# Kernel optimization log

Measured on AMD Instinct MI355X. Metric: run time of the kernel, lower is better.

The kernel has to match this reference:

```python
import jax, jax.numpy as jnp
import numpy as np

S_DIM = 128            # attention head width s
E_DIM = 1024           # expansion e = 2*hidden
SQRT_S = 128.0 ** 0.5
EPS = 1e-5


def setup_inputs() -> dict:
    key = jax.random.key(0)
    ks = jax.random.split(key, 8)
    B, S, H = 64, 512, 512
    uv_dim = 2 * E_DIM + S_DIM  # 2176
    # xavier-uniform-ish scale for uv weight
    lim = (6.0 / (H + uv_dim)) ** 0.5
    return {
        "x": jax.random.normal(ks[0], (B, S, H), dtype=jnp.float32),
        "ln_g": jnp.ones((1,), dtype=jnp.float32),
        "uv_w": jax.random.uniform(ks[1], (uv_dim, H), minval=-lim, maxval=lim, dtype=jnp.float32),
        "uv_b": jnp.zeros((uv_dim,), dtype=jnp.float32),
        "gamma": jax.random.uniform(ks[2], (2, S_DIM), dtype=jnp.float32),
        "beta": jax.random.uniform(ks[3], (2, S_DIM), dtype=jnp.float32),
        "w_bias": jax.random.uniform(ks[4], (2 * S - 1,), dtype=jnp.float32),
        "o_w": jax.random.normal(ks[5], (H, E_DIM), dtype=jnp.float32) * 0.02,
        "o_b": jnp.zeros((H,), dtype=jnp.float32),
    }


def _rope(x):
    # x: [B, S, 2, s]; rotate along the sequence dim (dim=1)
    S = x.shape[1]
    half = x.shape[-1] // 2
    pos = jnp.arange(S, dtype=jnp.float32)
    # torch: freq_seq = -arange(half)/half; inv_freq = 10000**(-freq_seq)
    inv_freq = 10000.0 ** (jnp.arange(half, dtype=jnp.float32) / half)
    sinus = pos[:, None, None] * inv_freq[None, None, :]  # [S, 1, half]
    sin, cos = jnp.sin(sinus), jnp.cos(sinus)
    x1, x2 = x[..., :half], x[..., half:]
    return jnp.concatenate([x1 * cos - x2 * sin, x2 * cos + x1 * sin], axis=-1)


def reference(x, ln_g, uv_w, uv_b, gamma, beta, w_bias, o_w, o_b):
    B, S, H = x.shape
    # ScaleNorm
    norm = jnp.linalg.norm(x, axis=-1, keepdims=True) * (H ** -0.5)
    xn = x / jnp.maximum(norm, EPS) * ln_g
    # fused uv projection + SiLU
    act = jax.nn.silu(xn @ uv_w.T + uv_b)  # [B, S, 2e+s]
    u = act[..., :E_DIM]
    v = act[..., E_DIM:2 * E_DIM]
    base = act[..., 2 * E_DIM:]                      # [B, S, s]
    base = base[:, :, None, :] * gamma + beta        # [B, S, 2, s]
    base = _rope(base)
    q, k = base[:, :, 0, :], base[:, :, 1, :]
    # scores + relative position bias: bias[i, j] = w[j - i + S - 1]
    qk = jnp.einsum('bsd,btd->bst', q, k)
    idx = jnp.arange(S)[None, :] - jnp.arange(S)[:, None] + (S - 1)
    qk = qk + w_bias[idx]
    # relu2 similarity kernel
    kernel = jnp.square(jax.nn.relu(qk / SQRT_S))    # [B, S, S]
    out = u * jnp.einsum('bst,bte->bse', kernel, v)  # gated attention
    out = out @ o_w.T + o_b
    return out + x  # use_shortcut: hidden == output
```

## Files before the change

kernel.cpp:

```cpp
#include <hip/hip_runtime.h>
#include <math.h>


#define M_TOT   32768
#define S_LEN   512
#define H_DIM   512
#define E_DIMC  1024
#define UV_DIM  2176
#define D_DIM   128

using floatx4  = __attribute__((ext_vector_type(4))) float;
using uintx2   = __attribute__((ext_vector_type(2))) unsigned int;
using uintx4   = __attribute__((ext_vector_type(4))) unsigned int;
using ushortx4 = __attribute__((ext_vector_type(4))) unsigned short;
using short8   = __attribute__((ext_vector_type(8))) short;

#define ASYNC_CP16(gsrc, ldst)                                                  \
    __builtin_amdgcn_global_load_lds(                                           \
        (const __attribute__((address_space(1))) void*)(gsrc),                  \
        (__attribute__((address_space(3))) void*)(ldst), 16, 0, 0)

__device__ __forceinline__ float bf2f(unsigned short h) {
    union { unsigned int u; float f; } c;
    c.u = ((unsigned int)h) << 16;
    return c.f;
}
__device__ __forceinline__ unsigned short f2bf(float f) {
    union { float f; unsigned int u; } c;
    c.f = f;
    unsigned int r = c.u + 0x7fffu + ((c.u >> 16) & 1u);
    return (unsigned short)(r >> 16);
}
__device__ __forceinline__ float silu_fast(float x) {
    float e = __expf(-x);
    return x * __builtin_amdgcn_rcpf(1.0f + e);
}

__global__ __launch_bounds__(256) void f2bf_kernel(const float* __restrict__ in,
                                                   unsigned short* __restrict__ out,
                                                   int n4) {
    int i = blockIdx.x * 256 + threadIdx.x;
    if (i < n4) {
        floatx4 v = ((const floatx4*)in)[i];
        ushortx4 o;
        o.x = f2bf(v.x); o.y = f2bf(v.y); o.z = f2bf(v.z); o.w = f2bf(v.w);
        ((ushortx4*)out)[i] = o;
    }
}

__global__ __launch_bounds__(256) void rmsnorm_kernel(const float* __restrict__ x,
                                                      const float* __restrict__ ln_g,
                                                      unsigned short* __restrict__ xn) {
    int row  = blockIdx.x * 4 + (threadIdx.x >> 6);
    int lane = threadIdx.x & 63;
    const float* xr = x + (size_t)row * H_DIM;
    floatx4 v0 = ((const floatx4*)xr)[lane];
    floatx4 v1 = ((const floatx4*)xr)[lane + 64];
    float ss = v0.x*v0.x + v0.y*v0.y + v0.z*v0.z + v0.w*v0.w
             + v1.x*v1.x + v1.y*v1.y + v1.z*v1.z + v1.w*v1.w;
    #pragma unroll
    for (int off = 32; off > 0; off >>= 1) ss += __shfl_xor(ss, off, 64);
    float norm = sqrtf(ss) * 0.044194173824159216f;
    float sc   = ln_g[0] / fmaxf(norm, 1e-5f);
    unsigned short* xo = xn + (size_t)row * H_DIM;
    ushortx4 o0, o1;
    o0.x = f2bf(v0.x * sc); o0.y = f2bf(v0.y * sc);
    o0.z = f2bf(v0.z * sc); o0.w = f2bf(v0.w * sc);
    o1.x = f2bf(v1.x * sc); o1.y = f2bf(v1.y * sc);
    o1.z = f2bf(v1.z * sc); o1.w = f2bf(v1.w * sc);
    ((ushortx4*)xo)[lane]      = o0;
    ((ushortx4*)xo)[lane + 64] = o1;
}

__global__ __launch_bounds__(64) void rope_table_kernel(float* __restrict__ cost,
                                                        float* __restrict__ sint) {
    int s = blockIdx.x;
    int j = threadIdx.x;
    float invf = (float)pow(10000.0, (double)j / 64.0);
    float ang  = (float)s * invf;
    double a   = (double)ang;
    cost[s * 64 + j] = (float)cos(a);
    sint[s * 64 + j] = (float)sin(a);
}

__global__ __launch_bounds__(256) void rope_apply_kernel(const float* __restrict__ base,
                                                         const float* __restrict__ gamma,
                                                         const float* __restrict__ beta,
                                                         const float* __restrict__ cost,
                                                         const float* __restrict__ sint,
                                                         unsigned short* __restrict__ q,
                                                         unsigned short* __restrict__ k) {
    int idx = blockIdx.x * 256 + threadIdx.x;
    int m = idx >> 6;
    int j = idx & 63;
    int s = m & (S_LEN - 1);
    float b1 = base[(size_t)m * D_DIM + j];
    float b2 = base[(size_t)m * D_DIM + 64 + j];
    float c  = cost[s * 64 + j];
    float sn = sint[s * 64 + j];
    float yq1 = b1 * gamma[j]       + beta[j];
    float yq2 = b2 * gamma[64 + j]  + beta[64 + j];
    float yk1 = b1 * gamma[128 + j] + beta[128 + j];
    float yk2 = b2 * gamma[192 + j] + beta[192 + j];
    q[(size_t)m * D_DIM + j]      = f2bf(yq1 * c - yq2 * sn);
    q[(size_t)m * D_DIM + 64 + j] = f2bf(yq2 * c + yq1 * sn);
    k[(size_t)m * D_DIM + j]      = f2bf(yk1 * c - yk2 * sn);
    k[(size_t)m * D_DIM + 64 + j] = f2bf(yk2 * c + yk1 * sn);
}

struct GemmLds {
    unsigned short As[128 * 64];
    unsigned short Bs[128 * 64];
};

template <bool SWAPT>
__device__ __forceinline__ void gemm_bt_core(const unsigned short* __restrict__ A,
                                             const unsigned short* __restrict__ B,
                                             int lda, int ldb, int K,
                                             int m0, int n0,
                                             GemmLds& lds, floatx4 (&acc)[4][4]) {
    const int tid  = threadIdx.x;
    const int lane = tid & 63;
    const int wave = tid >> 6;
    const int quad = lane >> 4;
    const int l16  = lane & 15;
    const int wm   = (wave >> 1) * 64;
    const int wn   = (wave & 1) * 64;
    const int lrow = lane >> 3;
    const int cgs  = ((lane & 7) ^ lrow) * 8;

    #pragma unroll
    for (int i = 0; i < 4; i++)
        #pragma unroll
        for (int j = 0; j < 4; j++) acc[i][j] = (floatx4){0.f, 0.f, 0.f, 0.f};

    for (int kt = 0; kt < K; kt += 64) {
        #pragma unroll
        for (int i = 0; i < 4; i++) {
            int r0 = wave * 32 + i * 8;
            const unsigned short* ga = A + (size_t)(m0 + r0 + lrow) * lda + kt + cgs;
            const unsigned short* gb = B + (size_t)(n0 + r0 + lrow) * ldb + kt + cgs;
            ASYNC_CP16(ga, &lds.As[r0 * 64]);
            ASYNC_CP16(gb, &lds.Bs[r0 * 64]);
        }
        __syncthreads();
        #pragma unroll
        for (int kk = 0; kk < 64; kk += 32) {
            short8 af[4], bf[4];
            const int pc = (kk + quad * 8) ^ ((l16 & 7) * 8);
            #pragma unroll
            for (int mt = 0; mt < 4; mt++) {
                int row = wm + mt * 16 + l16;
                union { short8 s8; uintx4 u4; } fu;
                fu.u4 = *(const uintx4*)&lds.As[row * 64 + pc];
                af[mt] = fu.s8;
            }
            #pragma unroll
            for (int nt = 0; nt < 4; nt++) {
                int row = wn + nt * 16 + l16;
                union { short8 s8; uintx4 u4; } fu;
                fu.u4 = *(const uintx4*)&lds.Bs[row * 64 + pc];
                bf[nt] = fu.s8;
            }
            #pragma unroll
            for (int mt = 0; mt < 4; mt++)
                #pragma unroll
                for (int nt = 0; nt < 4; nt++)
                    acc[mt][nt] = SWAPT
                        ? __builtin_amdgcn_mfma_f32_16x16x32_bf16(bf[nt], af[mt], acc[mt][nt], 0, 0, 0)
                        : __builtin_amdgcn_mfma_f32_16x16x32_bf16(af[mt], bf[nt], acc[mt][nt], 0, 0, 0);
        }
        __syncthreads();
    }
}

union LdsU {
    GemmLds g;
    unsigned short T[128 * 128];
};
__device__ __forceinline__ int swz(int row, int col) {
    return row * 128 + ((((col >> 3) ^ (row & 7)) << 3) | (col & 7));
}

__global__ __launch_bounds__(256) void gemm1_kernel(const unsigned short* __restrict__ xn,
                                                    const unsigned short* __restrict__ uvw,
                                                    const float* __restrict__ uvb,
                                                    unsigned short* __restrict__ u,
                                                    unsigned short* __restrict__ vT,
                                                    float* __restrict__ base) {
    __shared__ LdsU lds;
    floatx4 acc[4][4];
    const int m0 = blockIdx.x * 128, n0 = blockIdx.y * 128;

    const int tid = threadIdx.x, lane = tid & 63, wave = tid >> 6;
    const int quad = lane >> 4, l16 = lane & 15;
    const int wm = (wave >> 1) * 64, wn = (wave & 1) * 64;

    if (blockIdx.y < 8) {
        gemm_bt_core<true>(xn, uvw, H_DIM, H_DIM, H_DIM, m0, n0, lds.g, acc);
        #pragma unroll
        for (int mt = 0; mt < 4; mt++) {
            int row = wm + mt * 16 + l16;
            #pragma unroll
            for (int nt = 0; nt < 4; nt++) {
                int nl = wn + nt * 16 + quad * 4;
                floatx4 b4 = *(const floatx4*)&uvb[n0 + nl];
                ushortx4 pk;
                #pragma unroll
                for (int r = 0; r < 4; r++)
                    pk[r] = f2bf(silu_fast(acc[mt][nt][r] + b4[r]));
                *(uintx2*)&lds.T[swz(row, nl)] = *(uintx2*)&pk;
            }
        }
        __syncthreads();
        #pragma unroll
        for (int i = 0; i < 8; i++) {
            int idx = tid + i * 256;
            int row = idx >> 4;
            int j   = idx & 15;
            *(uintx4*)(u + (size_t)(m0 + row) * E_DIMC + n0 + j * 8) =
                *(const uintx4*)&lds.T[swz(row, j * 8)];
        }
    } else if (blockIdx.y < 16) {
        gemm_bt_core<false>(xn, uvw, H_DIM, H_DIM, H_DIM, m0, n0, lds.g, acc);
        #pragma unroll
        for (int nt = 0; nt < 4; nt++) {
            int nl = wn + nt * 16 + l16;
            float bias = uvb[n0 + nl];
            #pragma unroll
            for (int mt = 0; mt < 4; mt++) {
                ushortx4 pk;
                #pragma unroll
                for (int r = 0; r < 4; r++)
                    pk[r] = f2bf(silu_fast(acc[mt][nt][r] + bias));
                *(uintx2*)&lds.T[swz(nl, wm + mt * 16 + quad * 4)] = *(uintx2*)&pk;
            }
        }
        __syncthreads();
        const int b   = m0 >> 9;
        const int sg0 = m0 & (S_LEN - 1);
        const int eg0 = n0 - E_DIMC;
        #pragma unroll
        for (int i = 0; i < 8; i++) {
            int idx = tid + i * 256;
            int e   = idx >> 4;
            int j   = idx & 15;
            *(uintx4*)(vT + ((size_t)b * E_DIMC + eg0 + e) * S_LEN + sg0 + j * 8) =
                *(const uintx4*)&lds.T[swz(e, j * 8)];
        }
    } else {
        gemm_bt_core<false>(xn, uvw, H_DIM, H_DIM, H_DIM, m0, n0, lds.g, acc);
        #pragma unroll
        for (int mt = 0; mt < 4; mt++)
            #pragma unroll
            for (int nt = 0; nt < 4; nt++)
                #pragma unroll
                for (int r = 0; r < 4; r++) {
                    int m = m0 + wm + mt * 16 + quad * 4 + r;
                    int n = n0 + wn + nt * 16 + l16;
                    float val = acc[mt][nt][r] + uvb[n];
                    base[(size_t)m * D_DIM + (n - 2 * E_DIMC)] = silu_fast(val);
                }
    }
}

__global__ __launch_bounds__(256) void gemm_qk_kernel(const unsigned short* __restrict__ q,
                                                      const unsigned short* __restrict__ k,
                                                      const float* __restrict__ wbias,
                                                      unsigned short* __restrict__ P) {
    __shared__ LdsU lds;
    floatx4 acc[4][4];
    size_t boff = (size_t)blockIdx.z * S_LEN * D_DIM;
    unsigned short* Pb = P + (size_t)blockIdx.z * S_LEN * S_LEN;
    const int m0 = blockIdx.x * 128, n0 = blockIdx.y * 128;
    gemm_bt_core<true>(q + boff, k + boff, D_DIM, D_DIM, D_DIM, m0, n0, lds.g, acc);

    const int tid = threadIdx.x, lane = tid & 63, wave = tid >> 6;
    const int quad = lane >> 4, l16 = lane & 15;
    const int wm = (wave >> 1) * 64, wn = (wave & 1) * 64;
    #pragma unroll
    for (int mt = 0; mt < 4; mt++) {
        int row = wm + mt * 16 + l16;
        int s   = m0 + row;
        #pragma unroll
        for (int nt = 0; nt < 4; nt++) {
            int nl = wn + nt * 16 + quad * 4;
            int t0 = n0 + nl;
            ushortx4 pk;
            #pragma unroll
            for (int r = 0; r < 4; r++) {
                float z = (acc[mt][nt][r] + wbias[t0 + r - s + (S_LEN - 1)]) * 0.08838834764831845f;
                z = fmaxf(z, 0.f);
                pk[r] = f2bf(z * z);
            }
            *(uintx2*)&lds.T[swz(row, nl)] = *(uintx2*)&pk;
        }
    }
    __syncthreads();
    #pragma unroll
    for (int i = 0; i < 8; i++) {
        int idx = tid + i * 256;
        int row = idx >> 4;
        int j   = idx & 15;
        *(uintx4*)(Pb + (size_t)(m0 + row) * S_LEN + n0 + j * 8) =
            *(const uintx4*)&lds.T[swz(row, j * 8)];
    }
}

__global__ __launch_bounds__(256) void gemm_pv_kernel(const unsigned short* __restrict__ P,
                                                      const unsigned short* __restrict__ vT,
                                                      unsigned short* __restrict__ u) {
    __shared__ LdsU lds;
    floatx4 acc[4][4];
    int bb = blockIdx.z;
    const unsigned short* Pb  = P  + (size_t)bb * S_LEN * S_LEN;
    const unsigned short* vTb = vT + (size_t)bb * E_DIMC * S_LEN;
    const int m0 = blockIdx.x * 128, n0 = blockIdx.y * 128;
    gemm_bt_core<true>(Pb, vTb, S_LEN, S_LEN, S_LEN, m0, n0, lds.g, acc);

    const int tid = threadIdx.x, lane = tid & 63, wave = tid >> 6;
    const int quad = lane >> 4, l16 = lane & 15;
    const int wm = (wave >> 1) * 64, wn = (wave & 1) * 64;
    #pragma unroll
    for (int mt = 0; mt < 4; mt++) {
        int row = wm + mt * 16 + l16;
        #pragma unroll
        for (int nt = 0; nt < 4; nt++) {
            int nl = wn + nt * 16 + quad * 4;
            ushortx4 pk;
            #pragma unroll
            for (int r = 0; r < 4; r++) pk[r] = f2bf(acc[mt][nt][r]);
            *(uintx2*)&lds.T[swz(row, nl)] = *(uintx2*)&pk;
        }
    }
    __syncthreads();
    #pragma unroll
    for (int i = 0; i < 8; i++) {
        int idx = tid + i * 256;
        int row = idx >> 4;
        int j   = idx & 15;
        size_t off = ((size_t)bb * S_LEN + m0 + row) * E_DIMC + n0 + j * 8;
        union { uintx4 u4; unsigned short s[8]; } tv, uv, ov;
        tv.u4 = *(const uintx4*)&lds.T[swz(row, j * 8)];
        uv.u4 = *(const uintx4*)(u + off);
        #pragma unroll
        for (int jj = 0; jj < 8; jj++) ov.s[jj] = f2bf(bf2f(tv.s[jj]) * bf2f(uv.s[jj]));
        *(uintx4*)(u + off) = ov.u4;
    }
}

__global__ __launch_bounds__(256) void gemm_out_kernel(const unsigned short* __restrict__ oe,
                                                       const unsigned short* __restrict__ ow,
                                                       const float* __restrict__ ob,
                                                       const float* __restrict__ x,
                                                       float* __restrict__ out) {
    __shared__ GemmLds lds;
    floatx4 acc[4][4];
    const int m0 = blockIdx.y * 128, n0 = blockIdx.x * 128;
    gemm_bt_core<true>(oe, ow, E_DIMC, E_DIMC, E_DIMC, m0, n0, lds, acc);

    const int tid = threadIdx.x, lane = tid & 63, wave = tid >> 6;
    const int quad = lane >> 4, l16 = lane & 15;
    const int wm = (wave >> 1) * 64, wn = (wave & 1) * 64;

    #pragma unroll
    for (int mt = 0; mt < 4; mt++) {
        int m = m0 + wm + mt * 16 + l16;
        #pragma unroll
        for (int nt = 0; nt < 4; nt++) {
            int n = n0 + wn + nt * 16 + quad * 4;
            size_t off = (size_t)m * H_DIM + n;
            floatx4 b4 = *(const floatx4*)&ob[n];
            floatx4 x4 = *(const floatx4*)&x[off];
            *(floatx4*)&out[off] = acc[mt][nt] + b4 + x4;
        }
    }
}

extern "C" void kernel_launch(void* const* d_in, const int* in_sizes, int n_in,
                              void* d_out, int out_size, void* d_ws, size_t ws_size,
                              hipStream_t stream) {
    const float* x     = (const float*)d_in[0];
    const float* ln_g  = (const float*)d_in[1];
    const float* uv_w  = (const float*)d_in[2];
    const float* uv_b  = (const float*)d_in[3];
    const float* gamma = (const float*)d_in[4];
    const float* beta  = (const float*)d_in[5];
    const float* wbias = (const float*)d_in[6];
    const float* o_w   = (const float*)d_in[7];
    const float* o_b   = (const float*)d_in[8];
    float* out = (float*)d_out;

    char* ws = (char*)d_ws;
    size_t off = 0;
    auto alloc = [&](size_t bytes) {
        void* p = ws + off;
        off += (bytes + 255) & ~(size_t)255;
        return p;
    };
    unsigned short* u     = (unsigned short*)alloc((size_t)M_TOT * E_DIMC * 2);
    unsigned short* vT    = (unsigned short*)alloc((size_t)64 * E_DIMC * S_LEN * 2);
    unsigned short* xn    = (unsigned short*)alloc((size_t)M_TOT * H_DIM * 2);
    unsigned short* P     = xn;
    float*          base  = (float*)alloc((size_t)M_TOT * D_DIM * 4);
    unsigned short* q     = (unsigned short*)alloc((size_t)M_TOT * D_DIM * 2);
    unsigned short* k     = (unsigned short*)alloc((size_t)M_TOT * D_DIM * 2);
    float*          cost  = (float*)alloc((size_t)S_LEN * 64 * 4);
    float*          sint  = (float*)alloc((size_t)S_LEN * 64 * 4);
    unsigned short* uvwb  = (unsigned short*)alloc((size_t)UV_DIM * H_DIM * 2);
    unsigned short* owb   = (unsigned short*)alloc((size_t)H_DIM * E_DIMC * 2);
    (void)ws_size; (void)in_sizes; (void)n_in; (void)out_size;

    f2bf_kernel<<<(UV_DIM * H_DIM / 4 + 255) / 256, 256, 0, stream>>>(uv_w, uvwb, UV_DIM * H_DIM / 4);
    f2bf_kernel<<<(H_DIM * E_DIMC / 4 + 255) / 256, 256, 0, stream>>>(o_w, owb, H_DIM * E_DIMC / 4);
    rope_table_kernel<<<S_LEN, 64, 0, stream>>>(cost, sint);

    rmsnorm_kernel<<<M_TOT / 4, 256, 0, stream>>>(x, ln_g, xn);

    gemm1_kernel<<<dim3(M_TOT / 128, 17), 256, 0, stream>>>(xn, uvwb, uv_b, u, vT, base);

    rope_apply_kernel<<<M_TOT * 64 / 256, 256, 0, stream>>>(base, gamma, beta, cost, sint, q, k);

    gemm_qk_kernel<<<dim3(S_LEN / 128, S_LEN / 128, 64), 256, 0, stream>>>(q, k, wbias, P);

    gemm_pv_kernel<<<dim3(S_LEN / 128, E_DIMC / 128, 64), 256, 0, stream>>>(P, vT, u);

    gemm_out_kernel<<<dim3(H_DIM / 128, M_TOT / 128), 256, 0, stream>>>(u, owb, o_b, x, out);
}
```

Baseline: 398.9 us.

## Use 256x256 tiles with 4-stage async pipeline for projection GEMMs

Replaces the 128x128 uv-projection and output-projection GEMMs with 512-thread kernels computing 256x256 tiles. Each kernel uses a 4-buffer LDS ring filled by async global-to-LDS copies issued two k-steps ahead, plus raised wave priority around the MFMA bursts. The uv weight is zero-padded to 2304 rows so the final base tile fits the 256-wide grid. Larger tiles raise data reuse per LDS load, at the cost of far fewer blocks for the output GEMM (256) and wasted work on the padded base tile.

Result: no change. 393.7 us (-1.3%).

```diff
diff --git a/kernel.cpp b/kernel.cpp
--- a/kernel.cpp
+++ b/kernel.cpp
@@ -7,6 +7,7 @@
 #define H_DIM   512
 #define E_DIMC  1024
 #define UV_DIM  2176
+#define UV_PAD  2304
 #define D_DIM   128
 
 using floatx4  = __attribute__((ext_vector_type(4))) float;
@@ -44,6 +45,22 @@
         floatx4 v = ((const floatx4*)in)[i];
         ushortx4 o;
         o.x = f2bf(v.x); o.y = f2bf(v.y); o.z = f2bf(v.z); o.w = f2bf(v.w);
+        ((ushortx4*)out)[i] = o;
+    }
+}
+
+__global__ __launch_bounds__(256) void f2bf_pad_kernel(const float* __restrict__ in,
+                                                       unsigned short* __restrict__ out,
+                                                       int n4_src, int n4_dst) {
+    int i = blockIdx.x * 256 + threadIdx.x;
+    if (i < n4_dst) {
+        ushortx4 o;
+        if (i < n4_src) {
+            floatx4 v = ((const floatx4*)in)[i];
+            o.x = f2bf(v.x); o.y = f2bf(v.y); o.z = f2bf(v.z); o.w = f2bf(v.w);
+        } else {
+            o.x = 0; o.y = 0; o.z = 0; o.w = 0;
+        }
         ((ushortx4*)out)[i] = o;
     }
 }
@@ -108,6 +125,227 @@
     k[(size_t)m * D_DIM + 64 + j] = f2bf(yk2 * c + yk1 * sn);
 }
 
+template <bool SWAPT>
+__device__ __forceinline__ void gemm256_core(const unsigned short* __restrict__ A,
+                                             const unsigned short* __restrict__ B,
+                                             int lda, int ldb, int K,
+                                             int m0, int n0,
+                                             unsigned short (&st)[4][2][128][64],
+                                             floatx4 (&acc)[8][4]) {
+    const int tid  = threadIdx.x;
+    const int lane = tid & 63;
+    const int wave = tid >> 6;
+    const int quad = lane >> 4;
+    const int l16  = lane & 15;
+    const int wrow = (wave >> 2) * 128;
+    const int wcol = (wave & 3) * 64;
+
+    const int q0    = wave * 128 + lane;
+    const int R0    = q0 >> 3;
+    const int cp0   = q0 & 7;
+    const int c0    = cp0 ^ (R0 & 7);
+    const int srow0 = 2 * R0 + (c0 >> 2);
+    const int scol0 = (c0 & 3) * 8;
+
+    const unsigned short* pa0 = A + (size_t)(m0 + srow0) * lda + scol0;
+    const unsigned short* pa1 = pa0 + (size_t)16 * lda;
+    const unsigned short* pb0 = B + (size_t)(n0 + srow0) * ldb + scol0;
+    const unsigned short* pb1 = pb0 + (size_t)16 * ldb;
+    const int ldsOff0 = (wave * 128) * 8;
+    const int ldsOff1 = (wave * 128 + 64) * 8;
+
+    #pragma unroll
+    for (int i = 0; i < 8; i++)
+        #pragma unroll
+        for (int j = 0; j < 4; j++) acc[i][j] = (floatx4){0.f, 0.f, 0.f, 0.f};
+
+    const int NT = K >> 5;
+    auto stage = [&](int t) {
+        unsigned short* sA = &st[t & 3][0][0][0];
+        unsigned short* sB = &st[t & 3][1][0][0];
+        const int kt = t * 32;
+        ASYNC_CP16(pa0 + kt, sA + ldsOff0);
+        ASYNC_CP16(pa1 + kt, sA + ldsOff1);
+        ASYNC_CP16(pb0 + kt, sB + ldsOff0);
+        ASYNC_CP16(pb1 + kt, sB + ldsOff1);
+    };
+    stage(0);
+    stage(1);
+
+    int aoff[8], boff[4];
+    #pragma unroll
+    for (int mt = 0; mt < 8; mt++) {
+        int r  = wrow + mt * 16 + l16;
+        int Rr = r >> 1;
+        int cp = (((r & 1) << 2) + quad) ^ (Rr & 7);
+        aoff[mt] = Rr * 64 + cp * 8;
+    }
+    #pragma unroll
+    for (int nt = 0; nt < 4; nt++) {
+        int r  = wcol + nt * 16 + l16;
+        int Rr = r >> 1;
+        int cp = (((r & 1) << 2) + quad) ^ (Rr & 7);
+        boff[nt] = Rr * 64 + cp * 8;
+    }
+
+    for (int t = 0; t < NT; ++t) {
+        if (t < NT - 1) asm volatile("s_waitcnt vmcnt(4)" ::: "memory");
+        else            asm volatile("s_waitcnt vmcnt(0)" ::: "memory");
+        __builtin_amdgcn_sched_barrier(0);
+        __builtin_amdgcn_s_barrier();
+        __builtin_amdgcn_sched_barrier(0);
+        if (t + 2 < NT) stage(t + 2);
+
+        const unsigned short* sA = &st[t & 3][0][0][0];
+        const unsigned short* sB = &st[t & 3][1][0][0];
+        short8 bf[4];
+        #pragma unroll
+        for (int nt = 0; nt < 4; nt++) {
+            union { short8 s8; uintx4 u4; } fu;
+            fu.u4 = *(const uintx4*)&sB[boff[nt]];
+            bf[nt] = fu.s8;
+        }
+        #pragma unroll
+        for (int half = 0; half < 2; half++) {
+            short8 af[4];
+            #pragma unroll
+            for (int mt = 0; mt < 4; mt++) {
+                union { short8 s8; uintx4 u4; } fu;
+                fu.u4 = *(const uintx4*)&sA[aoff[half * 4 + mt]];
+                af[mt] = fu.s8;
+            }
+            __builtin_amdgcn_s_setprio(1);
+            #pragma unroll
+            for (int mt = 0; mt < 4; mt++)
+                #pragma unroll
+                for (int nt = 0; nt < 4; nt++)
+                    acc[half * 4 + mt][nt] = SWAPT
+                        ? __builtin_amdgcn_mfma_f32_16x16x32_bf16(bf[nt], af[mt], acc[half * 4 + mt][nt], 0, 0, 0)
+                        : __builtin_amdgcn_mfma_f32_16x16x32_bf16(af[mt], bf[nt], acc[half * 4 + mt][nt], 0, 0, 0);
+            __builtin_amdgcn_s_setprio(0);
+        }
+    }
+}
+
+union __align__(16) Lds256 {
+    unsigned short st[4][2][128][64];
+    unsigned short T[256 * 256];
+};
+
+__global__ __launch_bounds__(512, 2) void gemm1_256_kernel(const unsigned short* __restrict__ xn,
+                                                           const unsigned short* __restrict__ uvw,
+                                                           const float* __restrict__ uvb,
+                                                           unsigned short* __restrict__ u,
+                                                           unsigned short* __restrict__ vT,
+                                                           float* __restrict__ base) {
+    __shared__ Lds256 lds;
+    floatx4 acc[8][4];
+    const int m0 = blockIdx.y * 256;
+    const int xb = blockIdx.x;
+    const int tid = threadIdx.x, lane = tid & 63, wave = tid >> 6;
+    const int quad = lane >> 4, l16 = lane & 15;
+    const int wrow = (wave >> 2) * 128, wcol = (wave & 3) * 64;
+
+    if (xb < 4) {
+        const int n0 = xb * 256;
+        gemm256_core<true>(xn, uvw, H_DIM, H_DIM, H_DIM, m0, n0, lds.st, acc);
+        __syncthreads();
+        #pragma unroll
+        for (int mt = 0; mt < 8; mt++) {
+            int row = wrow + mt * 16 + l16;
+            #pragma unroll
+            for (int nt = 0; nt < 4; nt++) {
+                int nl = wcol + nt * 16 + quad * 4;
+                floatx4 b4 = *(const floatx4*)&uvb[n0 + nl];
+                ushortx4 pk;
+                #pragma unroll
+                for (int r = 0; r < 4; r++)
+                    pk[r] = f2bf(silu_fast(acc[mt][nt][r] + b4[r]));
+                *(uintx2*)&lds.T[row * 256 + (((nl >> 3) ^ (row & 15)) & 31) * 8 + (nl & 7)] = *(uintx2*)&pk;
+            }
+        }
+        __syncthreads();
+        #pragma unroll
+        for (int i = 0; i < 16; i++) {
+            int idx = tid + i * 512;
+            int row = idx >> 5, c16 = idx & 31;
+            *(uintx4*)(u + (size_t)(m0 + row) * E_DIMC + n0 + c16 * 8) =
+                *(const uintx4*)&lds.T[row * 256 + ((c16 ^ (row & 15)) * 8)];
+        }
+    } else if (xb < 8) {
+        const int n0 = xb * 256;
+        gemm256_core<false>(xn, uvw, H_DIM, H_DIM, H_DIM, m0, n0, lds.st, acc);
+        __syncthreads();
+        #pragma unroll
+        for (int nt = 0; nt < 4; nt++) {
+            int rowT = wcol + nt * 16 + l16;
+            float bias = uvb[n0 + rowT];
+            #pragma unroll
+            for (int mt = 0; mt < 8; mt++) {
+                int colT = wrow + mt * 16 + quad * 4;
+                ushortx4 pk;
+                #pragma unroll
+                for (int r = 0; r < 4; r++)
+                    pk[r] = f2bf(silu_fast(acc[mt][nt][r] + bias));
+                *(uintx2*)&lds.T[rowT * 256 + (((colT >> 3) ^ (rowT & 15)) & 31) * 8 + (colT & 7)] = *(uintx2*)&pk;
+            }
+        }
+        __syncthreads();
+        const int b = m0 >> 9, sg0 = m0 & (S_LEN - 1), eg0 = n0 - E_DIMC;
+        #pragma unroll
+        for (int i = 0; i < 16; i++) {
+            int idx = tid + i * 512;
+            int e = idx >> 5, c16 = idx & 31;
+            *(uintx4*)(vT + ((size_t)b * E_DIMC + eg0 + e) * S_LEN + sg0 + c16 * 8) =
+                *(const uintx4*)&lds.T[e * 256 + ((c16 ^ (e & 15)) * 8)];
+        }
+    } else {
+        const int n0 = 2048;
+        gemm256_core<false>(xn, uvw, H_DIM, H_DIM, H_DIM, m0, n0, lds.st, acc);
+        if ((wave & 3) < 2) {
+            #pragma unroll
+            for (int mt = 0; mt < 8; mt++) {
+                int m = m0 + wrow + mt * 16 + quad * 4;
+                #pragma unroll
+                for (int nt = 0; nt < 4; nt++) {
+                    int n = wcol + nt * 16 + l16;
+                    float bias = uvb[2048 + n];
+                    #pragma unroll
+                    for (int r = 0; r < 4; r++)
+                        base[(size_t)(m + r) * D_DIM + n] = silu_fast(acc[mt][nt][r] + bias);
+                }
+            }
+        }
+    }
+}
+
+__global__ __launch_bounds__(512, 2) void gemm_out256_kernel(const unsigned short* __restrict__ oe,
+                                                             const unsigned short* __restrict__ ow,
+                                                             const float* __restrict__ ob,
+                                                             const float* __restrict__ x,
+                                                             float* __restrict__ out) {
+    __shared__ __align__(16) unsigned short st[4][2][128][64];
+    floatx4 acc[8][4];
+    const int m0 = blockIdx.y * 256, n0 = blockIdx.x * 256;
+    gemm256_core<true>(oe, ow, E_DIMC, E_DIMC, E_DIMC, m0, n0, st, acc);
+
+    const int tid = threadIdx.x, lane = tid & 63, wave = tid >> 6;
+    const int quad = lane >> 4, l16 = lane & 15;
+    const int wrow = (wave >> 2) * 128, wcol = (wave & 3) * 64;
+    #pragma unroll
+    for (int mt = 0; mt < 8; mt++) {
+        int m = m0 + wrow + mt * 16 + l16;
+        #pragma unroll
+        for (int nt = 0; nt < 4; nt++) {
+            int n = n0 + wcol + nt * 16 + quad * 4;
+            size_t off = (size_t)m * H_DIM + n;
+            floatx4 b4 = *(const floatx4*)&ob[n];
+            floatx4 x4 = *(const floatx4*)&x[off];
+            *(floatx4*)&out[off] = acc[mt][nt] + b4 + x4;
+        }
+    }
+}
+
 struct GemmLds {
     unsigned short As[128 * 64];
     unsigned short Bs[128 * 64];
@@ -182,88 +420,6 @@
     return row * 128 + ((((col >> 3) ^ (row & 7)) << 3) | (col & 7));
 }
 
-__global__ __launch_bounds__(256) void gemm1_kernel(const unsigned short* __restrict__ xn,
-                                                    const unsigned short* __restrict__ uvw,
-                                                    const float* __restrict__ uvb,
-                                                    unsigned short* __restrict__ u,
-                                                    unsigned short* __restrict__ vT,
-                                                    float* __restrict__ base) {
-    __shared__ LdsU lds;
-    floatx4 acc[4][4];
-    const int m0 = blockIdx.x * 128, n0 = blockIdx.y * 128;
-
-    const int tid = threadIdx.x, lane = tid & 63, wave = tid >> 6;
-    const int quad = lane >> 4, l16 = lane & 15;
-    const int wm = (wave >> 1) * 64, wn = (wave & 1) * 64;
-
-    if (blockIdx.y < 8) {
-        gemm_bt_core<true>(xn, uvw, H_DIM, H_DIM, H_DIM, m0, n0, lds.g, acc);
-        #pragma unroll
-        for (int mt = 0; mt < 4; mt++) {
-            int row = wm + mt * 16 + l16;
-            #pragma unroll
-            for (int nt = 0; nt < 4; nt++) {
-                int nl = wn + nt * 16 + quad * 4;
-                floatx4 b4 = *(const floatx4*)&uvb[n0 + nl];
-                ushortx4 pk;
-                #pragma unroll
-                for (int r = 0; r < 4; r++)
-                    pk[r] = f2bf(silu_fast(acc[mt][nt][r] + b4[r]));
-                *(uintx2*)&lds.T[swz(row, nl)] = *(uintx2*)&pk;
-            }
-        }
-        __syncthreads();
-        #pragma unroll
-        for (int i = 0; i < 8; i++) {
-            int idx = tid + i * 256;
-            int row = idx >> 4;
-            int j   = idx & 15;
-            *(uintx4*)(u + (size_t)(m0 + row) * E_DIMC + n0 + j * 8) =
-                *(const uintx4*)&lds.T[swz(row, j * 8)];
-        }
-    } else if (blockIdx.y < 16) {
-        gemm_bt_core<false>(xn, uvw, H_DIM, H_DIM, H_DIM, m0, n0, lds.g, acc);
-        #pragma unroll
-        for (int nt = 0; nt < 4; nt++) {
-            int nl = wn + nt * 16 + l16;
-            float bias = uvb[n0 + nl];
-            #pragma unroll
-            for (int mt = 0; mt < 4; mt++) {
-                ushortx4 pk;
-                #pragma unroll
-                for (int r = 0; r < 4; r++)
-                    pk[r] = f2bf(silu_fast(acc[mt][nt][r] + bias));
-                *(uintx2*)&lds.T[swz(nl, wm + mt * 16 + quad * 4)] = *(uintx2*)&pk;
-            }
-        }
-        __syncthreads();
-        const int b   = m0 >> 9;
-        const int sg0 = m0 & (S_LEN - 1);
-        const int eg0 = n0 - E_DIMC;
-        #pragma unroll
-        for (int i = 0; i < 8; i++) {
-            int idx = tid + i * 256;
-            int e   = idx >> 4;
-            int j   = idx & 15;
-            *(uintx4*)(vT + ((size_t)b * E_DIMC + eg0 + e) * S_LEN + sg0 + j * 8) =
-                *(const uintx4*)&lds.T[swz(e, j * 8)];
-        }
-    } else {
-        gemm_bt_core<false>(xn, uvw, H_DIM, H_DIM, H_DIM, m0, n0, lds.g, acc);
-        #pragma unroll
-        for (int mt = 0; mt < 4; mt++)
-            #pragma unroll
-            for (int nt = 0; nt < 4; nt++)
-                #pragma unroll
-                for (int r = 0; r < 4; r++) {
-                    int m = m0 + wm + mt * 16 + quad * 4 + r;
-                    int n = n0 + wn + nt * 16 + l16;
-                    float val = acc[mt][nt][r] + uvb[n];
-                    base[(size_t)m * D_DIM + (n - 2 * E_DIMC)] = silu_fast(val);
-                }
-    }
-}
-
 __global__ __launch_bounds__(256) void gemm_qk_kernel(const unsigned short* __restrict__ q,
                                                       const unsigned short* __restrict__ k,
                                                       const float* __restrict__ wbias,
@@ -346,34 +502,6 @@
         #pragma unroll
         for (int jj = 0; jj < 8; jj++) ov.s[jj] = f2bf(bf2f(tv.s[jj]) * bf2f(uv.s[jj]));
         *(uintx4*)(u + off) = ov.u4;
-    }
-}
-
-__global__ __launch_bounds__(256) void gemm_out_kernel(const unsigned short* __restrict__ oe,
-                                                       const unsigned short* __restrict__ ow,
-                                                       const float* __restrict__ ob,
-                                                       const float* __restrict__ x,
-                                                       float* __restrict__ out) {
-    __shared__ GemmLds lds;
-    floatx4 acc[4][4];
-    const int m0 = blockIdx.y * 128, n0 = blockIdx.x * 128;
-    gemm_bt_core<true>(oe, ow, E_DIMC, E_DIMC, E_DIMC, m0, n0, lds, acc);
-
-    const int tid = threadIdx.x, lane = tid & 63, wave = tid >> 6;
-    const int quad = lane >> 4, l16 = lane & 15;
-    const int wm = (wave >> 1) * 64, wn = (wave & 1) * 64;
-
-    #pragma unroll
-    for (int mt = 0; mt < 4; mt++) {
-        int m = m0 + wm + mt * 16 + l16;
-        #pragma unroll
-        for (int nt = 0; nt < 4; nt++) {
-            int n = n0 + wn + nt * 16 + quad * 4;
-            size_t off = (size_t)m * H_DIM + n;
-            floatx4 b4 = *(const floatx4*)&ob[n];
-            floatx4 x4 = *(const floatx4*)&x[off];
-            *(floatx4*)&out[off] = acc[mt][nt] + b4 + x4;
-        }
     }
 }
 
@@ -407,17 +535,18 @@
     unsigned short* k     = (unsigned short*)alloc((size_t)M_TOT * D_DIM * 2);
     float*          cost  = (float*)alloc((size_t)S_LEN * 64 * 4);
     float*          sint  = (float*)alloc((size_t)S_LEN * 64 * 4);
-    unsigned short* uvwb  = (unsigned short*)alloc((size_t)UV_DIM * H_DIM * 2);
+    unsigned short* uvwb  = (unsigned short*)alloc((size_t)UV_PAD * H_DIM * 2);
     unsigned short* owb   = (unsigned short*)alloc((size_t)H_DIM * E_DIMC * 2);
     (void)ws_size; (void)in_sizes; (void)n_in; (void)out_size;
 
-    f2bf_kernel<<<(UV_DIM * H_DIM / 4 + 255) / 256, 256, 0, stream>>>(uv_w, uvwb, UV_DIM * H_DIM / 4);
+    f2bf_pad_kernel<<<(UV_PAD * H_DIM / 4 + 255) / 256, 256, 0, stream>>>(
+        uv_w, uvwb, UV_DIM * H_DIM / 4, UV_PAD * H_DIM / 4);
     f2bf_kernel<<<(H_DIM * E_DIMC / 4 + 255) / 256, 256, 0, stream>>>(o_w, owb, H_DIM * E_DIMC / 4);
     rope_table_kernel<<<S_LEN, 64, 0, stream>>>(cost, sint);
 
     rmsnorm_kernel<<<M_TOT / 4, 256, 0, stream>>>(x, ln_g, xn);
 
-    gemm1_kernel<<<dim3(M_TOT / 128, 17), 256, 0, stream>>>(xn, uvwb, uv_b, u, vT, base);
+    gemm1_256_kernel<<<dim3(9, M_TOT / 256), 512, 0, stream>>>(xn, uvwb, uv_b, u, vT, base);
 
     rope_apply_kernel<<<M_TOT * 64 / 256, 256, 0, stream>>>(base, gamma, beta, cost, sint, q, k);
 
@@ -425,5 +554,5 @@
 
     gemm_pv_kernel<<<dim3(S_LEN / 128, E_DIMC / 128, 64), 256, 0, stream>>>(P, vT, u);
 
-    gemm_out_kernel<<<dim3(H_DIM / 128, M_TOT / 128), 256, 0, stream>>>(u, owb, o_b, x, out);
-}
+    gemm_out256_kernel<<<dim3(H_DIM / 256, M_TOT / 256), 512, 0, stream>>>(u, owb, o_b, x, out);
+}
```
